# Performance work log

Measured on AMD Instinct MI355X. Metric: run time of the kernel, lower is better.

The kernel has to match this reference:

```python
import jax, jax.numpy as jnp
import numpy as np

F_DIM = 128; T = 3; N_RBF = 20; CUTOFF = 5.0; EPS = 1e-8
N_ATOMS = 10000; N_EDGES = 320000; N_MOL = 16; MAX_Z = 100


def setup_inputs():
    key = jax.random.key(0)
    ks = jax.random.split(key, 30)
    def w(k, shape, fan_in):
        return (jax.random.normal(k, shape, dtype=jnp.float32) / np.float32(np.sqrt(fan_in)))
    inp = {}
    inp["atomic_numbers"] = jax.random.randint(ks[0], (N_ATOMS,), 1, MAX_Z)
    inp["r_ij"] = jax.random.normal(ks[1], (N_EDGES, 3), dtype=jnp.float32) * 1.5
    inp["idx_i"] = jax.random.randint(ks[2], (N_EDGES,), 0, N_ATOMS)
    inp["idx_j"] = jax.random.randint(ks[3], (N_EDGES,), 0, N_ATOMS)
    inp["idx_m"] = jnp.sort(jax.random.randint(ks[4], (N_ATOMS,), 0, N_MOL))
    inp["e_field"] = jax.random.normal(ks[5], (N_MOL, 3), dtype=jnp.float32) * 0.1
    emb = jax.random.normal(ks[6], (MAX_Z, F_DIM), dtype=jnp.float32)
    inp["emb"] = emb.at[0].set(0.0)  # padding_idx=0
    inp["filt_W"] = w(ks[7], (N_RBF, T * 3 * F_DIM), N_RBF)
    inp["filt_b"] = jnp.zeros((T * 3 * F_DIM,), jnp.float32)
    inp["inter_W1"] = w(ks[8], (T, F_DIM, F_DIM), F_DIM)
    inp["inter_b1"] = jnp.zeros((T, F_DIM), jnp.float32)
    inp["inter_W2"] = w(ks[9], (T, F_DIM, 3 * F_DIM), F_DIM)
    inp["inter_b2"] = jnp.zeros((T, 3 * F_DIM), jnp.float32)
    inp["field_sW1"] = w(ks[10], (T, F_DIM, F_DIM), F_DIM)
    inp["field_sb1"] = jnp.zeros((T, F_DIM), jnp.float32)
    inp["field_sW2"] = w(ks[11], (T, F_DIM, F_DIM), F_DIM)
    inp["field_sb2"] = jnp.zeros((T, F_DIM), jnp.float32)
    inp["field_vW"] = w(ks[12], (T, F_DIM, F_DIM), F_DIM)
    inp["mix_muW"] = w(ks[13], (T, F_DIM, 2 * F_DIM), F_DIM)
    inp["mix_W1"] = w(ks[14], (T, 2 * F_DIM, F_DIM), 2 * F_DIM)
    inp["mix_b1"] = jnp.zeros((T, F_DIM), jnp.float32)
    inp["mix_W2"] = w(ks[15], (T, F_DIM, 3 * F_DIM), F_DIM)
    inp["mix_b2"] = jnp.zeros((T, 3 * F_DIM), jnp.float32)
    return inp


def _forward(r_ij, e_field, emb, filt_W, filt_b, inter_W1, inter_b1, inter_W2, inter_b2,
             field_sW1, field_sb1, field_sW2, field_sb2, field_vW,
             mix_muW, mix_W1, mix_b1, mix_W2, mix_b2,
             atomic_numbers, idx_i, idx_j, idx_m):
    silu = jax.nn.silu
    n_atoms = atomic_numbers.shape[0]
    # distances / directions
    d = jnp.sqrt(jnp.sum(r_ij * r_ij, axis=1, keepdims=True))        # [E,1]
    dir_ij = r_ij / d                                                # [E,3]
    # Gaussian RBF expansion
    offsets = jnp.linspace(0.0, CUTOFF, N_RBF, dtype=jnp.float32)
    width = offsets[1] - offsets[0]
    phi = jnp.exp(-0.5 * ((d[..., None] - offsets) / width) ** 2)    # [E,1,n_rbf]
    # cosine cutoff
    fcut = 0.5 * (jnp.cos(d * jnp.pi / CUTOFF) + 1.0) * (d < CUTOFF) # [E,1]
    filters = (phi @ filt_W + filt_b) * fcut[..., None]              # [E,1,T*3F]
    filter_list = jnp.split(filters, T, axis=-1)                     # T x [E,1,3F]
    q = emb[atomic_numbers][:, None, :]                              # [N,1,F]
    mu = jnp.zeros((n_atoms, 3, F_DIM), dtype=q.dtype)               # [N,3,F]
    E = e_field[idx_m][..., None]                                    # [N,3,1]
    for t in range(T):
        # --- PaiNNInteraction: edge message passing ---
        x = silu(q @ inter_W1[t] + inter_b1[t]) @ inter_W2[t] + inter_b2[t]  # [N,1,3F]
        xj = x[idx_j]                                                # [E,1,3F]
        muj = mu[idx_j]                                              # [E,3,F]
        xx = filter_list[t] * xj                                     # [E,1,3F]
        dq_e, dmuR, dmumu = jnp.split(xx, 3, axis=-1)                # [E,1,F] each
        dq = jax.ops.segment_sum(dq_e[:, 0, :], idx_i, num_segments=n_atoms)[:, None, :]
        dmu_e = dmuR * dir_ij[:, :, None] + dmumu * muj              # [E,3,F]
        dmu = jax.ops.segment_sum(dmu_e, idx_i, num_segments=n_atoms)
        q = q + dq
        mu = mu + dmu
        # --- FieldInteraction: pseudo-polarizability coupling ---
        a_s = silu(q @ field_sW1[t] + field_sb1[t]) @ field_sW2[t] + field_sb2[t]  # [N,1,F]
        a_v = mu @ field_vW[t]                                       # [N,3,F]
        mu = mu + a_s * E - jnp.sum(a_v * E, axis=1, keepdims=True) * a_v
        # --- PaiNNMixing: intra-atomic scalar/vector mixing ---
        mu_mix = mu @ mix_muW[t]                                     # [N,3,2F]
        mu_V, mu_Wc = jnp.split(mu_mix, 2, axis=-1)                  # [N,3,F]
        mu_Vn = jnp.sqrt(jnp.sum(mu_V ** 2, axis=-2, keepdims=True) + EPS)  # [N,1,F]
        ctx = jnp.concatenate([q, mu_Vn], axis=-1)                   # [N,1,2F]
        y = silu(ctx @ mix_W1[t] + mix_b1[t]) @ mix_W2[t] + mix_b2[t]  # [N,1,3F]
        dq_i, dmu_i, dqmu_i = jnp.split(y, 3, axis=-1)
        q = q + dq_i + dqmu_i * jnp.sum(mu_V * mu_Wc, axis=1, keepdims=True)
        mu = mu + dmu_i * mu_Wc
    # pack scalar (q [N,1,F]) and vector (mu [N,3,F]) reps into [N,4,F]
    return jnp.concatenate([q, mu], axis=1)


def reference(atomic_numbers, r_ij, idx_i, idx_j, idx_m, e_field, emb, filt_W, filt_b,
              inter_W1, inter_b1, inter_W2, inter_b2,
              field_sW1, field_sb1, field_sW2, field_sb2, field_vW,
              mix_muW, mix_W1, mix_b1, mix_W2, mix_b2):
    return _forward(r_ij, e_field, emb, filt_W, filt_b, inter_W1, inter_b1, inter_W2, inter_b2,
                    field_sW1, field_sb1, field_sW2, field_sb2, field_vW,
                    mix_muW, mix_W1, mix_b1, mix_W2, mix_b2,
                    atomic_numbers, idx_i, idx_j, idx_m)
```

## Files before the change

kernel.cpp:

```cpp
#include <hip/hip_runtime.h>

#define NA 10000
#define NE 320000

typedef short short8 __attribute__((ext_vector_type(8)));
typedef unsigned short us4 __attribute__((ext_vector_type(4)));
typedef float f32x4 __attribute__((ext_vector_type(4)));

__device__ __forceinline__ float silu_f(float v) { return v / (1.0f + __expf(-v)); }

__device__ __forceinline__ void split_bf16(float x, unsigned short& h, unsigned short& l)
{
    unsigned int u = __float_as_uint(x);
    h = (unsigned short)(u >> 16);
    float hf = __uint_as_float((unsigned int)h << 16);
    unsigned int ul = __float_as_uint(x - hf) + 0x8000u;
    l = (unsigned short)(ul >> 16);
}

__global__ __launch_bounds__(256) void k_init(
    const int* __restrict__ Z, const int* __restrict__ idx_m,
    const float* __restrict__ emb, const float* __restrict__ e_field,
    float* __restrict__ q, float* __restrict__ mu,
    float* __restrict__ Eat, int* __restrict__ counts, int* __restrict__ cursor)
{
    int gid = blockIdx.x * 256 + threadIdx.x;
    if (gid < NA * 384) mu[gid] = 0.0f;
    if (gid < NA * 128) {
        int i = gid >> 7, f = gid & 127;
        q[gid] = emb[Z[i] * 128 + f];
    }
    if (gid < NA * 3) {
        int i = gid / 3, d = gid - i * 3;
        Eat[gid] = e_field[idx_m[i] * 3 + d];
    }
    if (gid < NA) { counts[gid] = 0; cursor[gid] = 0; }
}

__global__ __launch_bounds__(256) void k_count(
    const int* __restrict__ idx_i, int* __restrict__ counts)
{
    int e = blockIdx.x * 256 + threadIdx.x;
    if (e < NE) atomicAdd(&counts[idx_i[e]], 1);
}

__global__ __launch_bounds__(256) void k_scan(const int* __restrict__ counts,
                                              int* __restrict__ rowptr)
{
    __shared__ int part[256];
    int tid = threadIdx.x;
    const int CH = (NA + 255) / 256;
    int base = tid * CH;
    int s = 0;
    for (int i2 = 0; i2 < CH; i2++) {
        int idx = base + i2;
        if (idx < NA) s += counts[idx];
    }
    part[tid] = s;
    __syncthreads();
    for (int ofs = 1; ofs < 256; ofs <<= 1) {
        int v = part[tid];
        int add = (tid >= ofs) ? part[tid - ofs] : 0;
        __syncthreads();
        part[tid] = v + add;
        __syncthreads();
    }
    int run = (tid > 0) ? part[tid - 1] : 0;
    for (int i2 = 0; i2 < CH; i2++) {
        int idx = base + i2;
        if (idx < NA) { rowptr[idx] = run; run += counts[idx]; }
        else if (idx == NA) rowptr[NA] = run;
    }
}

__global__ __launch_bounds__(256) void k_geom_scatter(
    const float* __restrict__ r_ij, const int* __restrict__ idx_i,
    const int* __restrict__ idx_j, const int* __restrict__ rowptr,
    int* __restrict__ cursor, float* __restrict__ phi_s,
    float4* __restrict__ df_s, int* __restrict__ j_s)
{
    int e = blockIdx.x * 256 + threadIdx.x;
    if (e >= NE) return;
    float x = r_ij[e*3+0], y = r_ij[e*3+1], z = r_ij[e*3+2];
    float d = sqrtf(x*x + y*y + z*z);
    float inv = 1.0f / d;
    float fc = (d < 5.0f) ? 0.5f * (__cosf(d * 0.628318530717958648f) + 1.0f) : 0.0f;
    int i = idx_i[e];
    int pos = rowptr[i] + atomicAdd(&cursor[i], 1);
    float4 dv; dv.x = x*inv; dv.y = y*inv; dv.z = z*inv; dv.w = fc;
    df_s[pos] = dv;
    j_s[pos] = idx_j[e];
    const float invw = 19.0f / 5.0f;
    float ph[20];
    #pragma unroll
    for (int k = 0; k < 20; k++) {
        float off = (5.0f / 19.0f) * (float)k;
        float u = (d - off) * invw;
        ph[k] = __expf(-0.5f * u * u) * fc;
    }
    #pragma unroll
    for (int c = 0; c < 5; c++) {
        float4 pv; pv.x = ph[c*4]; pv.y = ph[c*4+1]; pv.z = ph[c*4+2]; pv.w = ph[c*4+3];
        *(float4*)(phi_s + (size_t)pos*20 + c*4) = pv;
    }
}

struct WDesc { const float* src; unsigned short* dh; unsigned short* dl; int K; int N; };
struct WPack { WDesc w[24]; };

__global__ __launch_bounds__(256) void k_wprep(WPack P)
{
    WDesc d = P.w[blockIdx.y];
    int kBlks = d.K >> 5, nStrips = d.N >> 4;
    int total = nStrips * kBlks * 64;
    int g = blockIdx.x * 256 + threadIdx.x;
    if (g >= total) return;
    int lane = g & 63, rem = g >> 6;
    int kb = rem % kBlks, sIdx = rem / kBlks;
    int m16 = lane & 15, quad = lane >> 4;
    int n = sIdx * 16 + m16;
    int kbase = kb * 32 + quad * 8;
    size_t dofs = (size_t)g * 8;
    #pragma unroll
    for (int jj = 0; jj < 8; jj++) {
        unsigned short h, l;
        split_bf16(d.src[(size_t)(kbase + jj) * d.N + n], h, l);
        d.dh[dofs + jj] = h;
        d.dl[dofs + jj] = l;
    }
}

template<int ACT>
__global__ __launch_bounds__(256) void k_gmm2(
    const float* __restrict__ A,
    const unsigned short* __restrict__ Bh, const unsigned short* __restrict__ Bl,
    const float* __restrict__ bias, float* __restrict__ C,
    int M, int K, int N)
{
    __shared__ unsigned short Ahs[64 * 40];
    __shared__ unsigned short Als[64 * 40];
    int tid = threadIdx.x, lane = tid & 63, wv = tid >> 6;
    int i0 = blockIdx.x * 64, n0 = blockIdx.y * 64;
    int m16 = lane & 15, quad = lane >> 4;
    int kBlks = K >> 5;
    int sIdx = blockIdx.y * 4 + wv;

    f32x4 acc[4];
    #pragma unroll
    for (int a = 0; a < 4; a++) acc[a] = 0.0f;

    for (int kb = 0; kb < kBlks; kb++) {
        int k0 = kb << 5;
        __syncthreads();
        #pragma unroll
        for (int s = 0; s < 2; s++) {
            int idx = s * 256 + tid;
            int r = idx >> 3, c4 = (idx & 7) << 2;
            float4 v = {0.f, 0.f, 0.f, 0.f};
            if (i0 + r < M) v = *(const float4*)(A + (size_t)(i0 + r) * K + k0 + c4);
            unsigned short h0,l0,h1,l1,h2,l2,h3,l3;
            split_bf16(v.x, h0, l0); split_bf16(v.y, h1, l1);
            split_bf16(v.z, h2, l2); split_bf16(v.w, h3, l3);
            us4 hv = {h0, h1, h2, h3}, lv = {l0, l1, l2, l3};
            *(us4*)(Ahs + r * 40 + c4) = hv;
            *(us4*)(Als + r * 40 + c4) = lv;
        }
        __syncthreads();
        size_t bofs = (((size_t)sIdx * kBlks + kb) * 64 + lane) * 8;
        short8 bh = *(const short8*)(Bh + bofs);
        short8 bl = *(const short8*)(Bl + bofs);
        #pragma unroll
        for (int tm = 0; tm < 4; tm++) {
            short8 ah = *(const short8*)(Ahs + (tm * 16 + m16) * 40 + quad * 8);
            short8 al = *(const short8*)(Als + (tm * 16 + m16) * 40 + quad * 8);
            acc[tm] = __builtin_amdgcn_mfma_f32_16x16x32_bf16(ah, bh, acc[tm], 0, 0, 0);
            acc[tm] = __builtin_amdgcn_mfma_f32_16x16x32_bf16(ah, bl, acc[tm], 0, 0, 0);
            acc[tm] = __builtin_amdgcn_mfma_f32_16x16x32_bf16(al, bh, acc[tm], 0, 0, 0);
        }
    }
    int col = n0 + wv * 16 + m16;
    float bv = bias ? bias[col] : 0.0f;
    #pragma unroll
    for (int tm = 0; tm < 4; tm++) {
        #pragma unroll
        for (int r = 0; r < 4; r++) {
            int row = i0 + tm * 16 + quad * 4 + r;
            if (row < M) {
                float v = acc[tm][r] + bv;
                if (ACT) v = silu_f(v);
                C[(size_t)row * N + col] = v;
            }
        }
    }
}

template<int K1, int N2, int PRO, int EPI>
__global__ __launch_bounds__(256, 2) void k_mlp(
    const float* __restrict__ A, const float* __restrict__ mumix,
    const unsigned short* __restrict__ B1h, const unsigned short* __restrict__ B1l,
    const float* __restrict__ b1,
    const unsigned short* __restrict__ B2h, const unsigned short* __restrict__ B2l,
    const float* __restrict__ b2,
    float* __restrict__ C,
    const float* __restrict__ av, const float* __restrict__ Eat,
    float* __restrict__ qRW, float* __restrict__ muRW,
    float* __restrict__ outPk, int last, int M)
{
    const int KB1 = K1 / 32;
    const int S2  = N2 / 64;
    __shared__ unsigned short A1h[32 * 40];
    __shared__ unsigned short A1l[32 * 40];
    __shared__ unsigned short Hh[32 * 136];
    __shared__ unsigned short Hl[32 * 136];
    __shared__ float Ys[EPI == 2 ? 32 * 384 : 1];

    int tid = threadIdx.x, lane = tid & 63, wv = tid >> 6;
    int i0 = blockIdx.x * 32;
    int m16 = lane & 15, quad = lane >> 4;

    f32x4 acc1[2][2];
    #pragma unroll
    for (int s = 0; s < 2; s++)
        #pragma unroll
        for (int tm = 0; tm < 2; tm++) acc1[s][tm] = 0.0f;

    for (int kb = 0; kb < KB1; kb++) {
        int k0 = kb << 5;
        __syncthreads();
        {
            int r = tid >> 3, c4 = (tid & 7) << 2;
            int row = i0 + r;
            float4 v = {0.f, 0.f, 0.f, 0.f};
            if (row < M) {
                if (PRO == 0) {
                    v = *(const float4*)(A + (size_t)row * K1 + k0 + c4);
                } else {
                    int g = k0 + c4;
                    if (g < 128) {
                        v = *(const float4*)(A + (size_t)row * 128 + g);
                    } else {
                        int f = g - 128;
                        float4 v0 = *(const float4*)(mumix + ((size_t)row*3 + 0)*256 + f);
                        float4 v1 = *(const float4*)(mumix + ((size_t)row*3 + 1)*256 + f);
                        float4 v2 = *(const float4*)(mumix + ((size_t)row*3 + 2)*256 + f);
                        v.x = sqrtf(v0.x*v0.x + v1.x*v1.x + v2.x*v2.x + 1e-8f);
                        v.y = sqrtf(v0.y*v0.y + v1.y*v1.y + v2.y*v2.y + 1e-8f);
                        v.z = sqrtf(v0.z*v0.z + v1.z*v1.z + v2.z*v2.z + 1e-8f);
                        v.w = sqrtf(v0.w*v0.w + v1.w*v1.w + v2.w*v2.w + 1e-8f);
                    }
                }
            }
            unsigned short h0,l0,h1,l1,h2,l2,h3,l3;
            split_bf16(v.x, h0, l0); split_bf16(v.y, h1, l1);
            split_bf16(v.z, h2, l2); split_bf16(v.w, h3, l3);
            us4 hv = {h0, h1, h2, h3}, lv = {l0, l1, l2, l3};
            *(us4*)(A1h + r * 40 + c4) = hv;
            *(us4*)(A1l + r * 40 + c4) = lv;
        }
        __syncthreads();
        #pragma unroll
        for (int tm = 0; tm < 2; tm++) {
            short8 ah = *(const short8*)(A1h + (tm * 16 + m16) * 40 + quad * 8);
            short8 al = *(const short8*)(A1l + (tm * 16 + m16) * 40 + quad * 8);
            #pragma unroll
            for (int s = 0; s < 2; s++) {
                int sIdx = wv * 2 + s;
                size_t bofs = (((size_t)sIdx * KB1 + kb) * 64 + lane) * 8;
                short8 bh = *(const short8*)(B1h + bofs);
                short8 bl = *(const short8*)(B1l + bofs);
                acc1[s][tm] = __builtin_amdgcn_mfma_f32_16x16x32_bf16(ah, bh, acc1[s][tm], 0, 0, 0);
                acc1[s][tm] = __builtin_amdgcn_mfma_f32_16x16x32_bf16(ah, bl, acc1[s][tm], 0, 0, 0);
                acc1[s][tm] = __builtin_amdgcn_mfma_f32_16x16x32_bf16(al, bh, acc1[s][tm], 0, 0, 0);
            }
        }
    }
    __syncthreads();
    #pragma unroll
    for (int s = 0; s < 2; s++) {
        int col = wv * 32 + s * 16 + m16;
        float bb = b1[col];
        #pragma unroll
        for (int tm = 0; tm < 2; tm++) {
            #pragma unroll
            for (int r = 0; r < 4; r++) {
                int row = tm * 16 + quad * 4 + r;
                float v = silu_f(acc1[s][tm][r] + bb);
                unsigned short h, l;
                split_bf16(v, h, l);
                Hh[row * 136 + col] = h;
                Hl[row * 136 + col] = l;
            }
        }
    }
    __syncthreads();

    f32x4 acc2[S2][2];
    #pragma unroll
    for (int s = 0; s < S2; s++)
        #pragma unroll
        for (int tm = 0; tm < 2; tm++) acc2[s][tm] = 0.0f;

    #pragma unroll
    for (int kb = 0; kb < 4; kb++) {
        short8 ah[2], al[2];
        #pragma unroll
        for (int tm = 0; tm < 2; tm++) {
            ah[tm] = *(const short8*)(Hh + (tm * 16 + m16) * 136 + kb * 32 + quad * 8);
            al[tm] = *(const short8*)(Hl + (tm * 16 + m16) * 136 + kb * 32 + quad * 8);
        }
        #pragma unroll
        for (int s = 0; s < S2; s++) {
            int sIdx = wv * S2 + s;
            size_t bofs = (((size_t)sIdx * 4 + kb) * 64 + lane) * 8;
            short8 bh = *(const short8*)(B2h + bofs);
            short8 bl = *(const short8*)(B2l + bofs);
            #pragma unroll
            for (int tm = 0; tm < 2; tm++) {
                acc2[s][tm] = __builtin_amdgcn_mfma_f32_16x16x32_bf16(ah[tm], bh, acc2[s][tm], 0, 0, 0);
                acc2[s][tm] = __builtin_amdgcn_mfma_f32_16x16x32_bf16(ah[tm], bl, acc2[s][tm], 0, 0, 0);
                acc2[s][tm] = __builtin_amdgcn_mfma_f32_16x16x32_bf16(al[tm], bh, acc2[s][tm], 0, 0, 0);
            }
        }
    }

    if (EPI == 0) {
        #pragma unroll
        for (int s = 0; s < S2; s++) {
            int col = (wv * S2 + s) * 16 + m16;
            float bb = b2 ? b2[col] : 0.0f;
            #pragma unroll
            for (int tm = 0; tm < 2; tm++) {
                #pragma unroll
                for (int r = 0; r < 4; r++) {
                    int row = i0 + tm * 16 + quad * 4 + r;
                    if (row < M) C[(size_t)row * N2 + col] = acc2[s][tm][r] + bb;
                }
            }
        }
    } else if (EPI == 1) {
        #pragma unroll
        for (int s = 0; s < S2; s++) {
            int col = (wv * S2 + s) * 16 + m16;
            float bb = b2[col];
            #pragma unroll
            for (int tm = 0; tm < 2; tm++) {
                #pragma unroll
                for (int r = 0; r < 4; r++) {
                    int row = i0 + tm * 16 + quad * 4 + r;
                    if (row < M) {
                        float as = acc2[s][tm][r] + bb;
                        float E0 = Eat[row*3+0], E1 = Eat[row*3+1], E2 = Eat[row*3+2];
                        size_t b0 = ((size_t)row*3 + 0)*128 + col;
                        size_t b1o = ((size_t)row*3 + 1)*128 + col;
                        size_t b2o = ((size_t)row*3 + 2)*128 + col;
                        float a0 = av[b0], a1 = av[b1o], a2 = av[b2o];
                        float dot = a0*E0 + a1*E1 + a2*E2;
                        muRW[b0] += as*E0 - dot*a0;
                        muRW[b1o] += as*E1 - dot*a1;
                        muRW[b2o] += as*E2 - dot*a2;
                    }
                }
            }
        }
    } else {
        #pragma unroll
        for (int s = 0; s < S2; s++) {
            int col = (wv * S2 + s) * 16 + m16;
            float bb = b2[col];
            #pragma unroll
            for (int tm = 0; tm < 2; tm++) {
                #pragma unroll
                for (int r = 0; r < 4; r++) {
                    int row = tm * 16 + quad * 4 + r;
                    Ys[row * 384 + col] = acc2[s][tm][r] + bb;
                }
            }
        }
        __syncthreads();
        int f = tid & 127;
        #pragma unroll
        for (int it = 0; it < 16; it++) {
            int row = (tid >> 7) + it * 2;
            int i = i0 + row;
            if (i < M) {
                float yq  = Ys[row * 384 + f];
                float ym  = Ys[row * 384 + 128 + f];
                float yqm = Ys[row * 384 + 256 + f];
                float sdot = 0.0f;
                float W[3];
                #pragma unroll
                for (int d = 0; d < 3; d++) {
                    float Vd = mumix[((size_t)i*3 + d)*256 + f];
                    W[d]     = mumix[((size_t)i*3 + d)*256 + 128 + f];
                    sdot += Vd * W[d];
                }
                float qn = qRW[(size_t)i*128 + f] + yq + yqm * sdot;
                qRW[(size_t)i*128 + f] = qn;
                float mun[3];
                #pragma unroll
                for (int d = 0; d < 3; d++) {
                    size_t mo = ((size_t)i*3 + d)*128 + f;
                    mun[d] = muRW[mo] + ym * W[d];
                    muRW[mo] = mun[d];
                }
                if (last) {
                    outPk[(size_t)i*512 + f] = qn;
                    #pragma unroll
                    for (int d = 0; d < 3; d++)
                        outPk[(size_t)i*512 + 128 + d*128 + f] = mun[d];
                }
            }
        }
    }
}

__global__ __launch_bounds__(256, 3) void k_edge4(
    int t, const float* __restrict__ phi_s, const float4* __restrict__ df_s,
    const int* __restrict__ j_s, const int* __restrict__ rowptr,
    const float* __restrict__ x, const float* __restrict__ mu_in,
    const float* __restrict__ filt_W, const float* __restrict__ filt_b,
    float* __restrict__ q, float* __restrict__ mu_out)
{
    int lane = threadIdx.x & 63;
    int wv   = threadIdx.x >> 6;
    int ia   = blockIdx.x * 2 + (wv >> 1);
    int h    = wv & 1;
    int f    = lane + h * 64;

    float wreg[3][20];
    float b3[3];
    #pragma unroll
    for (int c = 0; c < 3; c++) {
        int col = t * 384 + (2*c + h) * 64 + lane;
        b3[c] = filt_b[col];
        #pragma unroll
        for (int k = 0; k < 20; k++)
            wreg[c][k] = filt_W[k * 1152 + col];
    }

    float accq = 0.0f, acc0 = 0.0f, acc1 = 0.0f, acc2 = 0.0f;
    int p0 = rowptr[ia], p1 = rowptr[ia + 1];
    int p = p0;
    for (; p + 4 <= p1; p += 4) {
        int jj[4]; float4 df[4];
        #pragma unroll
        for (int e = 0; e < 4; e++) { jj[e] = j_s[p + e]; df[e] = df_s[p + e]; }
        float dots[4][3];
        #pragma unroll
        for (int e = 0; e < 4; e++)
            #pragma unroll
            for (int c = 0; c < 3; c++) dots[e][c] = df[e].w * b3[c];
        #pragma unroll
        for (int kq = 0; kq < 5; kq++) {
            float4 a[4];
            #pragma unroll
            for (int e = 0; e < 4; e++)
                a[e] = *(const float4*)(phi_s + (size_t)(p + e) * 20 + kq * 4);
            #pragma unroll
            for (int e = 0; e < 4; e++) {
                #pragma unroll
                for (int c = 0; c < 3; c++) {
                    dots[e][c] = fmaf(a[e].x, wreg[c][kq*4+0], dots[e][c]);
                    dots[e][c] = fmaf(a[e].y, wreg[c][kq*4+1], dots[e][c]);
                    dots[e][c] = fmaf(a[e].z, wreg[c][kq*4+2], dots[e][c]);
                    dots[e][c] = fmaf(a[e].w, wreg[c][kq*4+3], dots[e][c]);
                }
            }
        }
        float xv[4][3], mv[4][3];
        #pragma unroll
        for (int e = 0; e < 4; e++) {
            size_t xb = (size_t)jj[e] * 384;
            xv[e][0] = x[xb + h*64 + lane];
            xv[e][1] = x[xb + (2+h)*64 + lane];
            xv[e][2] = x[xb + (4+h)*64 + lane];
            #pragma unroll
            for (int d = 0; d < 3; d++)
                mv[e][d] = mu_in[((size_t)jj[e]*3 + d)*128 + f];
        }
        #pragma unroll
        for (int e = 0; e < 4; e++) {
            float xxq = dots[e][0] * xv[e][0];
            float xxr = dots[e][1] * xv[e][1];
            float xxm = dots[e][2] * xv[e][2];
            accq += xxq;
            acc0 += xxr * df[e].x + xxm * mv[e][0];
            acc1 += xxr * df[e].y + xxm * mv[e][1];
            acc2 += xxr * df[e].z + xxm * mv[e][2];
        }
    }
    for (; p < p1; p++) {
        int j0 = j_s[p];
        float4 d0 = df_s[p];
        float dots0[3];
        #pragma unroll
        for (int c = 0; c < 3; c++) dots0[c] = d0.w * b3[c];
        #pragma unroll
        for (int kq = 0; kq < 5; kq++) {
            float4 a0 = *(const float4*)(phi_s + (size_t)p * 20 + kq * 4);
            #pragma unroll
            for (int c = 0; c < 3; c++) {
                dots0[c] = fmaf(a0.x, wreg[c][kq*4+0], dots0[c]);
                dots0[c] = fmaf(a0.y, wreg[c][kq*4+1], dots0[c]);
                dots0[c] = fmaf(a0.z, wreg[c][kq*4+2], dots0[c]);
                dots0[c] = fmaf(a0.w, wreg[c][kq*4+3], dots0[c]);
            }
        }
        size_t xb = (size_t)j0 * 384;
        float xq0 = x[xb + h*64 + lane];
        float xr0 = x[xb + (2+h)*64 + lane];
        float xm0 = x[xb + (4+h)*64 + lane];
        float m00 = mu_in[((size_t)j0*3 + 0)*128 + f];
        float m01 = mu_in[((size_t)j0*3 + 1)*128 + f];
        float m02 = mu_in[((size_t)j0*3 + 2)*128 + f];
        float xxq0 = dots0[0] * xq0, xxr0 = dots0[1] * xr0, xxm0 = dots0[2] * xm0;
        accq += xxq0;
        acc0 += xxr0*d0.x + xxm0*m00;
        acc1 += xxr0*d0.y + xxm0*m01;
        acc2 += xxr0*d0.z + xxm0*m02;
    }
    q[(size_t)ia*128 + f] += accq;
    mu_out[((size_t)ia*3 + 0)*128 + f] = mu_in[((size_t)ia*3 + 0)*128 + f] + acc0;
    mu_out[((size_t)ia*3 + 1)*128 + f] = mu_in[((size_t)ia*3 + 1)*128 + f] + acc1;
    mu_out[((size_t)ia*3 + 2)*128 + f] = mu_in[((size_t)ia*3 + 2)*128 + f] + acc2;
}

extern "C" void kernel_launch(void* const* d_in, const int* in_sizes, int n_in,
                              void* d_out, int out_size, void* d_ws, size_t ws_size,
                              hipStream_t stream)
{
    const int*   Z       = (const int*)d_in[0];
    const float* r_ij    = (const float*)d_in[1];
    const int*   idx_i   = (const int*)d_in[2];
    const int*   idx_j   = (const int*)d_in[3];
    const int*   idx_m   = (const int*)d_in[4];
    const float* e_field = (const float*)d_in[5];
    const float* emb     = (const float*)d_in[6];
    const float* filt_W  = (const float*)d_in[7];
    const float* filt_b  = (const float*)d_in[8];
    const float* iW1     = (const float*)d_in[9];
    const float* ib1     = (const float*)d_in[10];
    const float* iW2     = (const float*)d_in[11];
    const float* ib2     = (const float*)d_in[12];
    const float* sW1     = (const float*)d_in[13];
    const float* sb1     = (const float*)d_in[14];
    const float* sW2     = (const float*)d_in[15];
    const float* sb2     = (const float*)d_in[16];
    const float* vW      = (const float*)d_in[17];
    const float* mmW     = (const float*)d_in[18];
    const float* mW1     = (const float*)d_in[19];
    const float* mb1     = (const float*)d_in[20];
    const float* mW2     = (const float*)d_in[21];
    const float* mb2     = (const float*)d_in[22];
    float* out = (float*)d_out;

    float* base = (float*)d_ws;
    size_t off = 0;
    auto alloc = [&](size_t n) { float* p = base + off; off += (n + 255) & ~(size_t)255; return p; };
    float* q     = alloc((size_t)NA*128);
    float* mu_a  = alloc((size_t)NA*384);
    float* mu_b  = alloc((size_t)NA*384);
    float* s384  = alloc((size_t)NA*384);
    float* mumix = alloc((size_t)NA*768);
    float* Eat   = alloc((size_t)NA*3);
    float* phi_s = alloc((size_t)NE*20);
    float4* df_s = (float4*)alloc((size_t)NE*4);
    int* rowptr  = (int*)alloc(NA + 1);
    int* counts  = (int*)alloc(NA);
    int* cursor  = (int*)alloc(NA);
    int* j_s     = (int*)alloc(NE);
    unsigned short* wth = (unsigned short*)alloc(344064 + 256);
    unsigned short* wtl = (unsigned short*)alloc(344064 + 256);
    (void)ws_size; (void)in_sizes; (void)n_in; (void)out_size;

    WPack P;
    size_t woff = 0;
    unsigned short* WH[3][8];
    unsigned short* WL[3][8];
    int nw = 0;
    auto reg = [&](const float* src, int K, int N, int t, int slot) {
        P.w[nw].src = src; P.w[nw].dh = wth + woff; P.w[nw].dl = wtl + woff;
        P.w[nw].K = K; P.w[nw].N = N;
        WH[t][slot] = wth + woff; WL[t][slot] = wtl + woff;
        woff += (size_t)K * N; nw++;
    };
    for (int t = 0; t < 3; t++) {
        reg(iW1 + t*128*128, 128, 128, t, 0);
        reg(iW2 + t*128*384, 128, 384, t, 1);
        reg(sW1 + t*128*128, 128, 128, t, 2);
        reg(sW2 + t*128*128, 128, 128, t, 3);
        reg(vW  + t*128*128, 128, 128, t, 4);
        reg(mmW + t*128*256, 128, 256, t, 5);
        reg(mW1 + t*256*128, 256, 128, t, 6);
        reg(mW2 + t*128*384, 128, 384, t, 7);
    }

    k_wprep       <<<dim3(24, 24),          256, 0, stream>>>(P);
    k_init        <<<(NA*384 + 255)/256,    256, 0, stream>>>(Z, idx_m, emb, e_field, q, mu_a, Eat, counts, cursor);
    k_count       <<<(NE + 255)/256,        256, 0, stream>>>(idx_i, counts);
    k_scan        <<<1,                     256, 0, stream>>>(counts, rowptr);
    k_geom_scatter<<<(NE + 255)/256,        256, 0, stream>>>(r_ij, idx_i, idx_j, rowptr, cursor,
                                                              phi_s, df_s, j_s);

    const int G32   = (NA + 31) / 32;
    const int G64x3 = (NA*3 + 63) / 64;
    float* mu_cur = mu_a;
    float* mu_nxt = mu_b;
    for (int t = 0; t < 3; t++) {
        k_mlp<128,384,0,0><<<G32, 256, 0, stream>>>(
            q, nullptr, WH[t][0], WL[t][0], ib1 + t*128, WH[t][1], WL[t][1], ib2 + t*384,
            s384, nullptr, nullptr, nullptr, nullptr, nullptr, 0, NA);
        k_edge4<<<NA/2, 256, 0, stream>>>(t, phi_s, df_s, j_s, rowptr, s384,
                                          mu_cur, filt_W, filt_b, q, mu_nxt);
        { float* tmp = mu_cur; mu_cur = mu_nxt; mu_nxt = tmp; }
        k_gmm2<0><<<dim3(G64x3, 2), 256, 0, stream>>>(mu_cur, WH[t][4], WL[t][4], nullptr, s384, NA*3, 128, 128);
        k_mlp<128,128,0,1><<<G32, 256, 0, stream>>>(
            q, nullptr, WH[t][2], WL[t][2], sb1 + t*128, WH[t][3], WL[t][3], sb2 + t*128,
            nullptr, s384, Eat, nullptr, mu_cur, nullptr, 0, NA);
        k_gmm2<0><<<dim3(G64x3, 4), 256, 0, stream>>>(mu_cur, WH[t][5], WL[t][5], nullptr, mumix, NA*3, 128, 256);
        k_mlp<256,384,1,2><<<G32, 256, 0, stream>>>(
            q, mumix, WH[t][6], WL[t][6], mb1 + t*128, WH[t][7], WL[t][7], mb2 + t*384,
            nullptr, nullptr, nullptr, q, mu_cur, out, (t == 2) ? 1 : 0, NA);
    }
}
```

Baseline: 1.020 ms.

## Compute edge filter projections with split-bf16 MFMA in a wave-per-atom edge kernel

Replaces the scalar-FMA edge kernel with a 64-thread-per-block kernel. Each wave takes 16 edges at a time and computes the 20-RBF-to-384 filter projection as 16x16x32 bf16 MFMAs. The filter bias is folded in as an extra K column, and a three-term hi/lo bf16 split approximates fp32 accuracy. A new prep kernel pre-splits the filter weights and bias into bf16 hi/lo fragments in MFMA layout. The aim is to cut the per-edge scalar FMA work and the register-resident weight copies. In exchange, the neighbour gathers of x and mu now run in 16-lane segments, partial sums need cross-quad shuffle reductions, and the split-bf16 product may drift slightly from fp32.

```diff
diff --git a/kernel.cpp b/kernel.cpp
--- a/kernel.cpp
+++ b/kernel.cpp
@@ -127,6 +127,30 @@
         split_bf16(d.src[(size_t)(kbase + jj) * d.N + n], h, l);
         d.dh[dofs + jj] = h;
         d.dl[dofs + jj] = l;
+    }
+}
+
+__global__ __launch_bounds__(256) void k_wfprep(
+    const float* __restrict__ filt_W, const float* __restrict__ filt_b,
+    unsigned short* __restrict__ wfh, unsigned short* __restrict__ wfl)
+{
+    int g = blockIdx.x * 256 + threadIdx.x;
+    if (g >= 3 * 24 * 64) return;
+    int lane = g & 63, rem = g >> 6;
+    int st = rem % 24, t = rem / 24;
+    int col = lane & 15, quad = lane >> 4;
+    int tcol = t * 384 + st * 16 + col;
+    size_t dofs = (size_t)g * 8;
+    #pragma unroll
+    for (int j = 0; j < 8; j++) {
+        int k = quad * 8 + j;
+        float v = 0.0f;
+        if (k < 20) v = filt_W[k * 1152 + tcol];
+        else if (k == 20) v = filt_b[tcol];
+        unsigned short hh, ll;
+        split_bf16(v, hh, ll);
+        wfh[dofs + j] = hh;
+        wfl[dofs + j] = ll;
     }
 }
 
@@ -414,115 +438,120 @@
     }
 }
 
-__global__ __launch_bounds__(256, 3) void k_edge4(
+__global__ __launch_bounds__(64) void k_edgeM(
     int t, const float* __restrict__ phi_s, const float4* __restrict__ df_s,
     const int* __restrict__ j_s, const int* __restrict__ rowptr,
     const float* __restrict__ x, const float* __restrict__ mu_in,
-    const float* __restrict__ filt_W, const float* __restrict__ filt_b,
+    const unsigned short* __restrict__ wfh, const unsigned short* __restrict__ wfl,
     float* __restrict__ q, float* __restrict__ mu_out)
 {
-    int lane = threadIdx.x & 63;
-    int wv   = threadIdx.x >> 6;
-    int ia   = blockIdx.x * 2 + (wv >> 1);
-    int h    = wv & 1;
-    int f    = lane + h * 64;
-
-    float wreg[3][20];
-    float b3[3];
-    #pragma unroll
-    for (int c = 0; c < 3; c++) {
-        int col = t * 384 + (2*c + h) * 64 + lane;
-        b3[c] = filt_b[col];
-        #pragma unroll
-        for (int k = 0; k < 20; k++)
-            wreg[c][k] = filt_W[k * 1152 + col];
-    }
-
-    float accq = 0.0f, acc0 = 0.0f, acc1 = 0.0f, acc2 = 0.0f;
+    int lane = threadIdx.x;
+    int ia = blockIdx.x >> 1;
+    int h  = blockIdx.x & 1;
+    int col = lane & 15, quad = lane >> 4;
+
     int p0 = rowptr[ia], p1 = rowptr[ia + 1];
-    int p = p0;
-    for (; p + 4 <= p1; p += 4) {
-        int jj[4]; float4 df[4];
-        #pragma unroll
-        for (int e = 0; e < 4; e++) { jj[e] = j_s[p + e]; df[e] = df_s[p + e]; }
-        float dots[4][3];
-        #pragma unroll
-        for (int e = 0; e < 4; e++)
-            #pragma unroll
-            for (int c = 0; c < 3; c++) dots[e][c] = df[e].w * b3[c];
-        #pragma unroll
-        for (int kq = 0; kq < 5; kq++) {
-            float4 a[4];
-            #pragma unroll
-            for (int e = 0; e < 4; e++)
-                a[e] = *(const float4*)(phi_s + (size_t)(p + e) * 20 + kq * 4);
-            #pragma unroll
-            for (int e = 0; e < 4; e++) {
-                #pragma unroll
-                for (int c = 0; c < 3; c++) {
-                    dots[e][c] = fmaf(a[e].x, wreg[c][kq*4+0], dots[e][c]);
-                    dots[e][c] = fmaf(a[e].y, wreg[c][kq*4+1], dots[e][c]);
-                    dots[e][c] = fmaf(a[e].z, wreg[c][kq*4+2], dots[e][c]);
-                    dots[e][c] = fmaf(a[e].w, wreg[c][kq*4+3], dots[e][c]);
-                }
-            }
-        }
-        float xv[4][3], mv[4][3];
-        #pragma unroll
-        for (int e = 0; e < 4; e++) {
-            size_t xb = (size_t)jj[e] * 384;
-            xv[e][0] = x[xb + h*64 + lane];
-            xv[e][1] = x[xb + (2+h)*64 + lane];
-            xv[e][2] = x[xb + (4+h)*64 + lane];
-            #pragma unroll
-            for (int d = 0; d < 3; d++)
-                mv[e][d] = mu_in[((size_t)jj[e]*3 + d)*128 + f];
-        }
-        #pragma unroll
-        for (int e = 0; e < 4; e++) {
-            float xxq = dots[e][0] * xv[e][0];
-            float xxr = dots[e][1] * xv[e][1];
-            float xxm = dots[e][2] * xv[e][2];
-            accq += xxq;
-            acc0 += xxr * df[e].x + xxm * mv[e][0];
-            acc1 += xxr * df[e].y + xxm * mv[e][1];
-            acc2 += xxr * df[e].z + xxm * mv[e][2];
-        }
-    }
-    for (; p < p1; p++) {
-        int j0 = j_s[p];
-        float4 d0 = df_s[p];
-        float dots0[3];
-        #pragma unroll
-        for (int c = 0; c < 3; c++) dots0[c] = d0.w * b3[c];
-        #pragma unroll
-        for (int kq = 0; kq < 5; kq++) {
-            float4 a0 = *(const float4*)(phi_s + (size_t)p * 20 + kq * 4);
-            #pragma unroll
-            for (int c = 0; c < 3; c++) {
-                dots0[c] = fmaf(a0.x, wreg[c][kq*4+0], dots0[c]);
-                dots0[c] = fmaf(a0.y, wreg[c][kq*4+1], dots0[c]);
-                dots0[c] = fmaf(a0.z, wreg[c][kq*4+2], dots0[c]);
-                dots0[c] = fmaf(a0.w, wreg[c][kq*4+3], dots0[c]);
-            }
-        }
-        size_t xb = (size_t)j0 * 384;
-        float xq0 = x[xb + h*64 + lane];
-        float xr0 = x[xb + (2+h)*64 + lane];
-        float xm0 = x[xb + (4+h)*64 + lane];
-        float m00 = mu_in[((size_t)j0*3 + 0)*128 + f];
-        float m01 = mu_in[((size_t)j0*3 + 1)*128 + f];
-        float m02 = mu_in[((size_t)j0*3 + 2)*128 + f];
-        float xxq0 = dots0[0] * xq0, xxr0 = dots0[1] * xr0, xxm0 = dots0[2] * xm0;
-        accq += xxq0;
-        acc0 += xxr0*d0.x + xxm0*m00;
-        acc1 += xxr0*d0.y + xxm0*m01;
-        acc2 += xxr0*d0.z + xxm0*m02;
-    }
-    q[(size_t)ia*128 + f] += accq;
-    mu_out[((size_t)ia*3 + 0)*128 + f] = mu_in[((size_t)ia*3 + 0)*128 + f] + acc0;
-    mu_out[((size_t)ia*3 + 1)*128 + f] = mu_in[((size_t)ia*3 + 1)*128 + f] + acc1;
-    mu_out[((size_t)ia*3 + 2)*128 + f] = mu_in[((size_t)ia*3 + 2)*128 + f] + acc2;
+
+    float accq[4] = {};
+    float accd[3][4] = {};
+
+    for (int pb = p0; pb < p1; pb += 16) {
+        int e = pb + col;
+        bool val = (e < p1);
+        int ec = val ? e : (p1 - 1);
+        float av[8] = {0,0,0,0,0,0,0,0};
+        if (val) {
+            const float* pr = phi_s + (size_t)ec * 20;
+            if (quad == 0) {
+                float4 a = *(const float4*)(pr);
+                float4 b = *(const float4*)(pr + 4);
+                av[0]=a.x; av[1]=a.y; av[2]=a.z; av[3]=a.w;
+                av[4]=b.x; av[5]=b.y; av[6]=b.z; av[7]=b.w;
+            } else if (quad == 1) {
+                float4 a = *(const float4*)(pr + 8);
+                float4 b = *(const float4*)(pr + 12);
+                av[0]=a.x; av[1]=a.y; av[2]=a.z; av[3]=a.w;
+                av[4]=b.x; av[5]=b.y; av[6]=b.z; av[7]=b.w;
+            } else if (quad == 2) {
+                float4 a = *(const float4*)(pr + 16);
+                av[0]=a.x; av[1]=a.y; av[2]=a.z; av[3]=a.w;
+                av[4]=df_s[ec].w;
+            }
+        }
+        short8 ah, al;
+        #pragma unroll
+        for (int j = 0; j < 8; j++) {
+            unsigned short hh, ll;
+            split_bf16(av[j], hh, ll);
+            ah[j] = (short)hh; al[j] = (short)ll;
+        }
+
+        f32x4 dt[3][4];
+        #pragma unroll
+        for (int c = 0; c < 3; c++) {
+            #pragma unroll
+            for (int s = 0; s < 4; s++) {
+                int st = c * 8 + h * 4 + s;
+                size_t bo = (((size_t)(t * 24 + st)) * 64 + lane) * 8;
+                short8 bh = *(const short8*)(wfh + bo);
+                short8 bl = *(const short8*)(wfl + bo);
+                f32x4 d = {0.f, 0.f, 0.f, 0.f};
+                d = __builtin_amdgcn_mfma_f32_16x16x32_bf16(ah, bh, d, 0, 0, 0);
+                d = __builtin_amdgcn_mfma_f32_16x16x32_bf16(ah, bl, d, 0, 0, 0);
+                d = __builtin_amdgcn_mfma_f32_16x16x32_bf16(al, bh, d, 0, 0, 0);
+                dt[c][s] = d;
+            }
+        }
+
+        #pragma unroll
+        for (int r = 0; r < 4; r++) {
+            int pe = pb + quad * 4 + r;
+            if (pe > p1 - 1) pe = p1 - 1;
+            int j = j_s[pe];
+            float4 dfr = df_s[pe];
+            size_t xb = (size_t)j * 384 + h * 64 + col;
+            size_t mb = (size_t)j * 384 + h * 64 + col;
+            #pragma unroll
+            for (int s = 0; s < 4; s++) {
+                int o = s * 16;
+                float xq  = x[xb + o];
+                float xr_ = x[xb + 128 + o];
+                float xm  = x[xb + 256 + o];
+                float m0  = mu_in[mb + o];
+                float m1  = mu_in[mb + 128 + o];
+                float m2  = mu_in[mb + 256 + o];
+                accq[s]    += dt[0][s][r] * xq;
+                float xxr = dt[1][s][r] * xr_;
+                float xxm = dt[2][s][r] * xm;
+                accd[0][s] += xxr * dfr.x + xxm * m0;
+                accd[1][s] += xxr * dfr.y + xxm * m1;
+                accd[2][s] += xxr * dfr.z + xxm * m2;
+            }
+        }
+    }
+
+    #pragma unroll
+    for (int s = 0; s < 4; s++) {
+        accq[s] += __shfl_xor(accq[s], 16);
+        accq[s] += __shfl_xor(accq[s], 32);
+        #pragma unroll
+        for (int d = 0; d < 3; d++) {
+            accd[d][s] += __shfl_xor(accd[d][s], 16);
+            accd[d][s] += __shfl_xor(accd[d][s], 32);
+        }
+    }
+    if (quad == 0) {
+        #pragma unroll
+        for (int s = 0; s < 4; s++) {
+            size_t qo = (size_t)ia * 128 + h * 64 + s * 16 + col;
+            q[qo] += accq[s];
+            #pragma unroll
+            for (int d = 0; d < 3; d++) {
+                size_t mo = ((size_t)ia * 3 + d) * 128 + h * 64 + s * 16 + col;
+                mu_out[mo] = mu_in[mo] + accd[d][s];
+            }
+        }
+    }
 }
 
 extern "C" void kernel_launch(void* const* d_in, const int* in_sizes, int n_in,
@@ -571,6 +600,8 @@
     int* j_s     = (int*)alloc(NE);
     unsigned short* wth = (unsigned short*)alloc(344064 + 256);
     unsigned short* wtl = (unsigned short*)alloc(344064 + 256);
+    unsigned short* wfh = (unsigned short*)alloc(3*24*64*8/2 + 256);
+    unsigned short* wfl = (unsigned short*)alloc(3*24*64*8/2 + 256);
     (void)ws_size; (void)in_sizes; (void)n_in; (void)out_size;
 
     WPack P;
@@ -596,6 +627,7 @@
     }
 
     k_wprep       <<<dim3(24, 24),          256, 0, stream>>>(P);
+    k_wfprep      <<<18,                    256, 0, stream>>>(filt_W, filt_b, wfh, wfl);
     k_init        <<<(NA*384 + 255)/256,    256, 0, stream>>>(Z, idx_m, emb, e_field, q, mu_a, Eat, counts, cursor);
     k_count       <<<(NE + 255)/256,        256, 0, stream>>>(idx_i, counts);
     k_scan        <<<1,                     256, 0, stream>>>(counts, rowptr);
@@ -610,8 +642,8 @@
         k_mlp<128,384,0,0><<<G32, 256, 0, stream>>>(
             q, nullptr, WH[t][0], WL[t][0], ib1 + t*128, WH[t][1], WL[t][1], ib2 + t*384,
             s384, nullptr, nullptr, nullptr, nullptr, nullptr, 0, NA);
-        k_edge4<<<NA/2, 256, 0, stream>>>(t, phi_s, df_s, j_s, rowptr, s384,
-                                          mu_cur, filt_W, filt_b, q, mu_nxt);
+        k_edgeM<<<NA*2, 64, 0, stream>>>(t, phi_s, df_s, j_s, rowptr, s384,
+                                         mu_cur, wfh, wfl, q, mu_nxt);
         { float* tmp = mu_cur; mu_cur = mu_nxt; mu_nxt = tmp; }
         k_gmm2<0><<<dim3(G64x3, 2), 256, 0, stream>>>(mu_cur, WH[t][4], WL[t][4], nullptr, s384, NA*3, 128, 128);
         k_mlp<128,128,0,1><<<G32, 256, 0, stream>>>(
```

Result: slower. 1.512 ms (+48.3%).
